# Kernel optimization log

Hardware: AMD Instinct MI355X
Metric: run time of the kernel (lower is better)

## Reference

```python
import jax, jax.numpy as jnp
import numpy as np

N_NODES = 100000


def _gcn_layer(x, src, dst, nrm, W, b):
    # x: [N, Din] -> [N, Dout]. GCNConv: linear transform then deg-normalized scatter-add.
    h = x @ W                                  # [N, Dout]
    msg = h[src] * nrm[:, None]               # gather + per-edge normalization, [E', Dout]
    agg = jax.ops.segment_sum(msg, dst, num_segments=N_NODES)
    return agg + b


def setup_inputs() -> dict:
    key = jax.random.key(0)
    ks = jax.random.split(key, 16)
    x = jax.random.normal(ks[0], (N_NODES, 128), dtype=jnp.float32)
    edge_index = jax.random.randint(ks[1], (2, 1600000), 0, N_NODES, dtype=jnp.int64)
    d = {"x": x, "edge_index": edge_index}
    dims = [(128, 64), (64, 64), (64, 64), (64, 64), (64, 64), (64, 64)]
    for i, (din, dout) in enumerate(dims):
        scale = 1.0 / np.sqrt(din)
        d[f"W{i+1}"] = jax.random.uniform(ks[2 + 2 * i], (din, dout), jnp.float32, -scale, scale)
        d[f"b{i+1}"] = jnp.zeros((dout,), jnp.float32)
    return d


def reference(x, edge_index, W1, b1, W2, b2, W3, b3, W4, b4, W5, b5, W6, b6):
    # Add self-loops (GCNConv default), symmetric normalization D^-1/2 A D^-1/2.
    loops = jnp.arange(N_NODES, dtype=edge_index.dtype)
    src = jnp.concatenate([edge_index[0], loops])
    dst = jnp.concatenate([edge_index[1], loops])
    deg = jax.ops.segment_sum(jnp.ones_like(dst, dtype=x.dtype), dst, num_segments=N_NODES)
    dinv = jnp.where(deg > 0, jax.lax.rsqrt(deg), 0.0)
    nrm = dinv[src] * dinv[dst]               # per-edge norm coefficient, [E']

    h = x
    for (W, b) in ((W1, b1), (W2, b2), (W3, b3), (W4, b4), (W5, b5), (W6, b6)):
        h = jax.nn.relu(_gcn_layer(h, src, dst, nrm, W, b))
        # eval mode: dropout is identity
    return jax.nn.log_softmax(h, axis=-1)
```

## Files before the change

### kernel.cpp

```cpp
#include <hip/hip_runtime.h>
#include <hip/hip_fp16.h>
#include <math.h>

#define N_NODES 100000
#define N_EDGES 1600000
#define NB 1563
#define CAP 2048
#define NBLK_S 128
#define CHUNK (N_EDGES / NBLK_S)

typedef _Float16 half8_t __attribute__((ext_vector_type(8)));
typedef float floatx4 __attribute__((ext_vector_type(4)));


__global__ __launch_bounds__(1024) void k_hist(const int* __restrict__ dst,
                                               int* __restrict__ ghist) {
    __shared__ int hist[NB];
    int blk = blockIdx.x, t = threadIdx.x;
    for (int i = t; i < NB; i += 1024) hist[i] = 0;
    __syncthreads();
    const int4* dq = (const int4*)(dst + blk * CHUNK);
    const int nq = CHUNK >> 2;
    for (int i = t; i < nq; i += 1024) {
        int4 d = dq[i];
        atomicAdd(&hist[d.x >> 6], 1);
        atomicAdd(&hist[d.y >> 6], 1);
        atomicAdd(&hist[d.z >> 6], 1);
        atomicAdd(&hist[d.w >> 6], 1);
    }
    __syncthreads();
    for (int i = t; i < NB; i += 1024) ghist[i * NBLK_S + blk] = hist[i];
}

__global__ void k_scanb(int* __restrict__ ghist, int* __restrict__ btot) {
    __shared__ int s[NBLK_S];
    int b = blockIdx.x, t = threadIdx.x;
    int v = ghist[b * NBLK_S + t];
    s[t] = v;
    __syncthreads();
    for (int off = 1; off < NBLK_S; off <<= 1) {
        int a = (t >= off) ? s[t - off] : 0;
        __syncthreads();
        s[t] += a;
        __syncthreads();
    }
    ghist[b * NBLK_S + t] = s[t] - v;
    if (t == NBLK_S - 1) btot[b] = s[t];
}

__global__ void k_scant(const int* __restrict__ btot, int* __restrict__ bbase,
                        int* __restrict__ rowptr) {
    __shared__ int s[1024];
    __shared__ int carry;
    int t = threadIdx.x;
    if (t == 0) carry = 0;
    __syncthreads();
    for (int chunk = 0; chunk < 2; ++chunk) {
        int i = chunk * 1024 + t;
        int v = (i < NB) ? btot[i] : 0;
        s[t] = v;
        __syncthreads();
        for (int off = 1; off < 1024; off <<= 1) {
            int a = (t >= off) ? s[t - off] : 0;
            __syncthreads();
            s[t] += a;
            __syncthreads();
        }
        if (i < NB) bbase[i] = carry + s[t] - v;
        int total = carry + s[1023];
        __syncthreads();
        if (t == 0) carry = total;
        __syncthreads();
    }
    if (t == 0) rowptr[N_NODES] = N_EDGES;
}

__global__ __launch_bounds__(1024) void k_scatter(const int* __restrict__ src,
                                                  const int* __restrict__ dst,
                                                  const int* __restrict__ ghist,
                                                  const int* __restrict__ bbase,
                                                  unsigned* __restrict__ bentry) {
    __shared__ int cursor[NB];
    int blk = blockIdx.x, t = threadIdx.x;
    for (int i = t; i < NB; i += 1024)
        cursor[i] = bbase[i] + ghist[i * NBLK_S + blk];
    __syncthreads();
    const int4* dq = (const int4*)(dst + blk * CHUNK);
    const int4* sq = (const int4*)(src + blk * CHUNK);
    const int nq = CHUNK >> 2;
    for (int i = t; i < nq; i += 1024) {
        int4 d = dq[i];
        int4 s = sq[i];
        int p0 = atomicAdd(&cursor[d.x >> 6], 1);
        int p1 = atomicAdd(&cursor[d.y >> 6], 1);
        int p2 = atomicAdd(&cursor[d.z >> 6], 1);
        int p3 = atomicAdd(&cursor[d.w >> 6], 1);
        bentry[p0] = ((unsigned)(d.x & 63) << 17) | (unsigned)s.x;
        bentry[p1] = ((unsigned)(d.y & 63) << 17) | (unsigned)s.y;
        bentry[p2] = ((unsigned)(d.z & 63) << 17) | (unsigned)s.z;
        bentry[p3] = ((unsigned)(d.w & 63) << 17) | (unsigned)s.w;
    }
}

__global__ __launch_bounds__(256) void k_fill2(const int* __restrict__ btot,
                                               const int* __restrict__ bbase,
                                               const unsigned* __restrict__ bentry,
                                               int* __restrict__ rowptr,
                                               float* __restrict__ dinv,
                                               int* __restrict__ colv) {
    __shared__ unsigned ent[CAP];
    __shared__ int hist[64];
    __shared__ int cursor[64];
    int b = blockIdx.x;
    int t = threadIdx.x;
    int cnt = btot[b]; if (cnt > CAP) cnt = CAP;
    int base = bbase[b];
    if (t < 64) hist[t] = 0;
    __syncthreads();
    const unsigned* be = bentry + base;
    for (int i = t; i < cnt; i += 256) {
        unsigned e = be[i];
        ent[i] = e;
        atomicAdd(&hist[e >> 17], 1);
    }
    __syncthreads();
    if (t < 64) {
        int v = hist[t];
        int incl = v;
#pragma unroll
        for (int off = 1; off < 64; off <<= 1) {
            int a = __shfl_up(incl, off);
            if (t >= off) incl += a;
        }
        int excl = incl - v;
        cursor[t] = excl;
        int node = (b << 6) + t;
        if (node < N_NODES) {
            rowptr[node] = base + excl;
            dinv[node] = rsqrtf((float)(v + 1));
        }
    }
    __syncthreads();
    for (int i = t; i < cnt; i += 256) {
        unsigned e = ent[i];
        int pos = base + atomicAdd(&cursor[e >> 17], 1);
        colv[pos] = (int)(e & 0x1FFFF);
    }
}


__global__ void k_prepw(const float* __restrict__ W1, const float* __restrict__ W2,
                        const float* __restrict__ W3, const float* __restrict__ W4,
                        const float* __restrict__ W5, const float* __restrict__ W6,
                        __half* __restrict__ wt) {
    int l = blockIdx.x;
    const float* W = (l == 0) ? W1 : (l == 1) ? W2 : (l == 2) ? W3
                   : (l == 3) ? W4 : (l == 4) ? W5 : W6;
    int din = (l == 0) ? 128 : 64;
    __half* dstp = wt + ((l == 0) ? 0 : 8192 + (l - 1) * 4096);
    int n = 64 * din;
    for (int i = threadIdx.x; i < n; i += blockDim.x) {
        int col = i / din, k = i - col * din;
        dstp[i] = __float2half(W[k * 64 + col]);
    }
}


template<int DIN, int F32IN>
__global__ __launch_bounds__(256) void k_gemm(const void* __restrict__ in,
                                              const __half* __restrict__ Wt,
                                              const float* __restrict__ dinv,
                                              __half* __restrict__ h) {
    int tid  = threadIdx.x;
    int lane = tid & 63;
    int node0 = blockIdx.x * 64 + (tid >> 6) * 16;
    if (node0 >= N_NODES) return;
    int lr = lane & 15;
    int lk = (lane >> 4) * 8;

    int arow = node0 + lr; if (arow >= N_NODES) arow = N_NODES - 1;
    const __half* ap  = (const __half*)in + (size_t)arow * DIN + lk;
    const float*  ap32 = (const float*)in + (size_t)arow * DIN + lk;
    const __half* bp = Wt + (size_t)lr * DIN + lk;

    floatx4 acc0 = {0.f, 0.f, 0.f, 0.f}, acc1 = acc0, acc2 = acc0, acc3 = acc0;
#pragma unroll
    for (int kc = 0; kc < DIN / 32; ++kc) {
        half8_t a;
        if (F32IN) {
            float4 f0 = *(const float4*)(ap32 + kc * 32);
            float4 f1 = *(const float4*)(ap32 + kc * 32 + 4);
            a[0] = (_Float16)f0.x; a[1] = (_Float16)f0.y;
            a[2] = (_Float16)f0.z; a[3] = (_Float16)f0.w;
            a[4] = (_Float16)f1.x; a[5] = (_Float16)f1.y;
            a[6] = (_Float16)f1.z; a[7] = (_Float16)f1.w;
        } else {
            a = *(const half8_t*)(ap + kc * 32);
        }
        half8_t b0 = *(const half8_t*)(bp + kc * 32);
        half8_t b1 = *(const half8_t*)(bp + kc * 32 + 16 * DIN);
        half8_t b2 = *(const half8_t*)(bp + kc * 32 + 32 * DIN);
        half8_t b3 = *(const half8_t*)(bp + kc * 32 + 48 * DIN);
        acc0 = __builtin_amdgcn_mfma_f32_16x16x32_f16(a, b0, acc0, 0, 0, 0);
        acc1 = __builtin_amdgcn_mfma_f32_16x16x32_f16(a, b1, acc1, 0, 0, 0);
        acc2 = __builtin_amdgcn_mfma_f32_16x16x32_f16(a, b2, acc2, 0, 0, 0);
        acc3 = __builtin_amdgcn_mfma_f32_16x16x32_f16(a, b3, acc3, 0, 0, 0);
    }

    int rbase = node0 + (lane >> 4) * 4;
#pragma unroll
    for (int r = 0; r < 4; ++r) {
        int row = rbase + r;
        if (row < N_NODES) {
            float dn = dinv[row];
            __half* op = h + ((size_t)row << 6) + lr;
            op[0]  = __float2half(acc0[r] * dn);
            op[16] = __float2half(acc1[r] * dn);
            op[32] = __float2half(acc2[r] * dn);
            op[48] = __float2half(acc3[r] * dn);
        }
    }
}


template<int LAST>
__global__ __launch_bounds__(256) void k_aggregate(const int* __restrict__ rowptr,
                                                   const int* __restrict__ colv,
                                                   const __half* __restrict__ h,
                                                   const float* __restrict__ dinv,
                                                   const float* __restrict__ bias,
                                                   __half* __restrict__ acta,
                                                   float* __restrict__ outf) {
    int tid  = threadIdx.x;
    int node = blockIdx.x * 16 + (tid >> 4);
    if (node >= N_NODES) return;
    int ql = tid & 15;

    int beg = rowptr[node], end = rowptr[node + 1];
    const __half* hp = h + (ql << 2);

    __half2 z = __floats2half2_rn(0.f, 0.f);
    __half2 A0 = z, A1 = z, B0 = z, B1 = z, C0 = z, C1 = z, D0 = z, D1 = z;
    union UV { uint2 u; __half2 h2[2]; };
    int k = beg;
    for (; k + 8 <= end; k += 8) {
        int s0 = colv[k],     s1 = colv[k + 1], s2 = colv[k + 2], s3 = colv[k + 3];
        int s4 = colv[k + 4], s5 = colv[k + 5], s6 = colv[k + 6], s7 = colv[k + 7];
        UV v0, v1, v2, v3, v4, v5, v6, v7;
        v0.u = *(const uint2*)(hp + ((size_t)s0 << 6));
        v1.u = *(const uint2*)(hp + ((size_t)s1 << 6));
        v2.u = *(const uint2*)(hp + ((size_t)s2 << 6));
        v3.u = *(const uint2*)(hp + ((size_t)s3 << 6));
        v4.u = *(const uint2*)(hp + ((size_t)s4 << 6));
        v5.u = *(const uint2*)(hp + ((size_t)s5 << 6));
        v6.u = *(const uint2*)(hp + ((size_t)s6 << 6));
        v7.u = *(const uint2*)(hp + ((size_t)s7 << 6));
        A0 = __hadd2(A0, v0.h2[0]); A1 = __hadd2(A1, v0.h2[1]);
        B0 = __hadd2(B0, v1.h2[0]); B1 = __hadd2(B1, v1.h2[1]);
        C0 = __hadd2(C0, v2.h2[0]); C1 = __hadd2(C1, v2.h2[1]);
        D0 = __hadd2(D0, v3.h2[0]); D1 = __hadd2(D1, v3.h2[1]);
        A0 = __hadd2(A0, v4.h2[0]); A1 = __hadd2(A1, v4.h2[1]);
        B0 = __hadd2(B0, v5.h2[0]); B1 = __hadd2(B1, v5.h2[1]);
        C0 = __hadd2(C0, v6.h2[0]); C1 = __hadd2(C1, v6.h2[1]);
        D0 = __hadd2(D0, v7.h2[0]); D1 = __hadd2(D1, v7.h2[1]);
    }
    for (; k + 4 <= end; k += 4) {
        int s0 = colv[k], s1 = colv[k + 1], s2 = colv[k + 2], s3 = colv[k + 3];
        UV v0, v1, v2, v3;
        v0.u = *(const uint2*)(hp + ((size_t)s0 << 6));
        v1.u = *(const uint2*)(hp + ((size_t)s1 << 6));
        v2.u = *(const uint2*)(hp + ((size_t)s2 << 6));
        v3.u = *(const uint2*)(hp + ((size_t)s3 << 6));
        A0 = __hadd2(A0, v0.h2[0]); A1 = __hadd2(A1, v0.h2[1]);
        B0 = __hadd2(B0, v1.h2[0]); B1 = __hadd2(B1, v1.h2[1]);
        C0 = __hadd2(C0, v2.h2[0]); C1 = __hadd2(C1, v2.h2[1]);
        D0 = __hadd2(D0, v3.h2[0]); D1 = __hadd2(D1, v3.h2[1]);
    }
    for (; k < end; ++k) {
        int s0 = colv[k];
        UV v0;
        v0.u = *(const uint2*)(hp + ((size_t)s0 << 6));
        A0 = __hadd2(A0, v0.h2[0]); A1 = __hadd2(A1, v0.h2[1]);
    }
    A0 = __hadd2(__hadd2(A0, B0), __hadd2(C0, D0));
    A1 = __hadd2(__hadd2(A1, B1), __hadd2(C1, D1));

    float2 f0 = __half22float2(A0), f1 = __half22float2(A1);
    UV sv;
    sv.u = *(const uint2*)(hp + ((size_t)node << 6));
    float2 s0f = __half22float2(sv.h2[0]), s1f = __half22float2(sv.h2[1]);
    float dn = dinv[node];
    float4 bv = ((const float4*)bias)[ql];
    float r0 = fmaxf(fmaf(f0.x + s0f.x, dn, bv.x), 0.f);
    float r1 = fmaxf(fmaf(f0.y + s0f.y, dn, bv.y), 0.f);
    float r2 = fmaxf(fmaf(f1.x + s1f.x, dn, bv.z), 0.f);
    float r3 = fmaxf(fmaf(f1.y + s1f.y, dn, bv.w), 0.f);

    if (LAST) {
        float m = fmaxf(fmaxf(r0, r1), fmaxf(r2, r3));
#pragma unroll
        for (int off = 1; off <= 8; off <<= 1) m = fmaxf(m, __shfl_xor(m, off));
        float ss = expf(r0 - m) + expf(r1 - m) + expf(r2 - m) + expf(r3 - m);
#pragma unroll
        for (int off = 1; off <= 8; off <<= 1) ss += __shfl_xor(ss, off);
        float lse = m + logf(ss);
        *(float4*)(outf + ((size_t)node << 6) + (ql << 2)) =
            make_float4(r0 - lse, r1 - lse, r2 - lse, r3 - lse);
    } else {
        UV pk;
        pk.h2[0] = __floats2half2_rn(r0, r1);
        pk.h2[1] = __floats2half2_rn(r2, r3);
        *(uint2*)(acta + ((size_t)node << 6) + (ql << 2)) = pk.u;
    }
}


extern "C" void kernel_launch(void* const* d_in, const int* in_sizes, int n_in,
                              void* d_out, int out_size, void* d_ws, size_t ws_size,
                              hipStream_t stream) {
    const float* x = (const float*)d_in[0];
    const int* ei  = (const int*)d_in[1];
    const int* src = ei;
    const int* dst = ei + N_EDGES;

    const float* W[6];
    const float* b[6];
    for (int i = 0; i < 6; ++i) {
        W[i] = (const float*)d_in[2 + 2 * i];
        b[i] = (const float*)d_in[3 + 2 * i];
    }
    float* out = (float*)d_out;

    char* p = (char*)d_ws;
    __half* h      = (__half*)p; p += (size_t)N_NODES * 64 * 2;
    __half* act    = (__half*)p; p += (size_t)N_NODES * 64 * 2;
    __half* wt     = (__half*)p; p += 28672 * 2;
    int*    rowptr = (int*)p;    p += (size_t)(N_NODES + 1) * 4;
    float*  dinv   = (float*)p;  p += (size_t)N_NODES * 4;
    int*    colv   = (int*)p;
    unsigned* bentry = (unsigned*)h;
    int*    ghist = (int*)(bentry + (size_t)N_EDGES);
    int*    btot  = ghist + (size_t)NB * NBLK_S;
    int*    bbase = btot + NB;

    const int nb_q    = (N_NODES + 15) / 16;
    const int nb_tile = (N_NODES + 63) / 64;

    k_prepw<<<6, 256, 0, stream>>>(W[0], W[1], W[2], W[3], W[4], W[5], wt);

    k_hist<<<NBLK_S, 1024, 0, stream>>>(dst, ghist);
    k_scanb<<<NB, NBLK_S, 0, stream>>>(ghist, btot);
    k_scant<<<1, 1024, 0, stream>>>(btot, bbase, rowptr);
    k_scatter<<<NBLK_S, 1024, 0, stream>>>(src, dst, ghist, bbase, bentry);
    k_fill2<<<NB, 256, 0, stream>>>(btot, bbase, bentry, rowptr, dinv, colv);

    for (int l = 0; l < 6; ++l) {
        if (l == 0)
            k_gemm<128, 1><<<nb_tile, 256, 0, stream>>>(x, wt, dinv, h);
        else
            k_gemm<64, 0><<<nb_tile, 256, 0, stream>>>(act, wt + 8192 + (l - 1) * 4096, dinv, h);
        if (l == 5)
            k_aggregate<1><<<nb_q, 256, 0, stream>>>(rowptr, colv, h, dinv, b[l], act, out);
        else
            k_aggregate<0><<<nb_q, 256, 0, stream>>>(rowptr, colv, h, dinv, b[l], act, out);
    }
}
```

Before: 351.5 us.

## Fuse aggregation of layer l with GEMM of layer l+1 via LDS tile

Each layer's neighbor aggregation (with bias, ReLU and fp16 packing) now writes a 64-node tile into shared memory, and the next layer's MFMA GEMM reads it from there, all in one kernel. This drops the intermediate activation write/read through global memory and five kernel launches, using ping-pong h buffers. The cost is fewer, larger blocks (64 nodes each, 4 serial node rows per 16-lane group), which lowers parallelism for latency hiding in the gather.

Result: slower. 366.8 us (+4.4%).

```diff
diff --git a/kernel.cpp b/kernel.cpp
--- a/kernel.cpp
+++ b/kernel.cpp
@@ -166,11 +166,10 @@
 }
 
 
-template<int DIN, int F32IN>
-__global__ __launch_bounds__(256) void k_gemm(const void* __restrict__ in,
-                                              const __half* __restrict__ Wt,
-                                              const float* __restrict__ dinv,
-                                              __half* __restrict__ h) {
+__global__ __launch_bounds__(256) void k_gemm0(const float* __restrict__ in,
+                                               const __half* __restrict__ Wt,
+                                               const float* __restrict__ dinv,
+                                               __half* __restrict__ h) {
     int tid  = threadIdx.x;
     int lane = tid & 63;
     int node0 = blockIdx.x * 64 + (tid >> 6) * 16;
@@ -179,28 +178,23 @@
     int lk = (lane >> 4) * 8;
 
     int arow = node0 + lr; if (arow >= N_NODES) arow = N_NODES - 1;
-    const __half* ap  = (const __half*)in + (size_t)arow * DIN + lk;
-    const float*  ap32 = (const float*)in + (size_t)arow * DIN + lk;
-    const __half* bp = Wt + (size_t)lr * DIN + lk;
+    const float*  ap32 = in + (size_t)arow * 128 + lk;
+    const __half* bp = Wt + (size_t)lr * 128 + lk;
 
     floatx4 acc0 = {0.f, 0.f, 0.f, 0.f}, acc1 = acc0, acc2 = acc0, acc3 = acc0;
 #pragma unroll
-    for (int kc = 0; kc < DIN / 32; ++kc) {
+    for (int kc = 0; kc < 4; ++kc) {
+        float4 f0 = *(const float4*)(ap32 + kc * 32);
+        float4 f1 = *(const float4*)(ap32 + kc * 32 + 4);
         half8_t a;
-        if (F32IN) {
-            float4 f0 = *(const float4*)(ap32 + kc * 32);
-            float4 f1 = *(const float4*)(ap32 + kc * 32 + 4);
-            a[0] = (_Float16)f0.x; a[1] = (_Float16)f0.y;
-            a[2] = (_Float16)f0.z; a[3] = (_Float16)f0.w;
-            a[4] = (_Float16)f1.x; a[5] = (_Float16)f1.y;
-            a[6] = (_Float16)f1.z; a[7] = (_Float16)f1.w;
-        } else {
-            a = *(const half8_t*)(ap + kc * 32);
-        }
+        a[0] = (_Float16)f0.x; a[1] = (_Float16)f0.y;
+        a[2] = (_Float16)f0.z; a[3] = (_Float16)f0.w;
+        a[4] = (_Float16)f1.x; a[5] = (_Float16)f1.y;
+        a[6] = (_Float16)f1.z; a[7] = (_Float16)f1.w;
         half8_t b0 = *(const half8_t*)(bp + kc * 32);
-        half8_t b1 = *(const half8_t*)(bp + kc * 32 + 16 * DIN);
-        half8_t b2 = *(const half8_t*)(bp + kc * 32 + 32 * DIN);
-        half8_t b3 = *(const half8_t*)(bp + kc * 32 + 48 * DIN);
+        half8_t b1 = *(const half8_t*)(bp + kc * 32 + 16 * 128);
+        half8_t b2 = *(const half8_t*)(bp + kc * 32 + 32 * 128);
+        half8_t b3 = *(const half8_t*)(bp + kc * 32 + 48 * 128);
         acc0 = __builtin_amdgcn_mfma_f32_16x16x32_f16(a, b0, acc0, 0, 0, 0);
         acc1 = __builtin_amdgcn_mfma_f32_16x16x32_f16(a, b1, acc1, 0, 0, 0);
         acc2 = __builtin_amdgcn_mfma_f32_16x16x32_f16(a, b2, acc2, 0, 0, 0);
@@ -223,14 +217,130 @@
 }
 
 
-template<int LAST>
-__global__ __launch_bounds__(256) void k_aggregate(const int* __restrict__ rowptr,
-                                                   const int* __restrict__ colv,
-                                                   const __half* __restrict__ h,
-                                                   const float* __restrict__ dinv,
-                                                   const float* __restrict__ bias,
-                                                   __half* __restrict__ acta,
-                                                   float* __restrict__ outf) {
+__global__ __launch_bounds__(256) void k_fused(const int* __restrict__ rowptr,
+                                               const int* __restrict__ colv,
+                                               const __half* __restrict__ h,
+                                               const float* __restrict__ dinv,
+                                               const float* __restrict__ bias,
+                                               const __half* __restrict__ Wt,
+                                               __half* __restrict__ hn) {
+    __shared__ __half sA[64 * 80];
+    int tid = threadIdx.x;
+    int node0 = blockIdx.x * 64;
+    int q = tid >> 4, ql = tid & 15;
+    const __half* hp = h + (ql << 2);
+    float4 bv = ((const float4*)bias)[ql];
+    union UV { uint2 u; __half2 h2[2]; };
+
+    for (int j = 0; j < 4; ++j) {
+        int trow = (j << 4) + q;
+        int node = node0 + trow;
+        uint2* sdst = (uint2*)&sA[trow * 80 + (ql << 2)];
+        if (node >= N_NODES) { *sdst = make_uint2(0u, 0u); continue; }
+        int beg = rowptr[node], end = rowptr[node + 1];
+        __half2 z = __floats2half2_rn(0.f, 0.f);
+        __half2 A0 = z, A1 = z, B0 = z, B1 = z, C0 = z, C1 = z, D0 = z, D1 = z;
+        int k = beg;
+        for (; k + 8 <= end; k += 8) {
+            int s0 = colv[k],     s1 = colv[k + 1], s2 = colv[k + 2], s3 = colv[k + 3];
+            int s4 = colv[k + 4], s5 = colv[k + 5], s6 = colv[k + 6], s7 = colv[k + 7];
+            UV v0, v1, v2, v3, v4, v5, v6, v7;
+            v0.u = *(const uint2*)(hp + ((size_t)s0 << 6));
+            v1.u = *(const uint2*)(hp + ((size_t)s1 << 6));
+            v2.u = *(const uint2*)(hp + ((size_t)s2 << 6));
+            v3.u = *(const uint2*)(hp + ((size_t)s3 << 6));
+            v4.u = *(const uint2*)(hp + ((size_t)s4 << 6));
+            v5.u = *(const uint2*)(hp + ((size_t)s5 << 6));
+            v6.u = *(const uint2*)(hp + ((size_t)s6 << 6));
+            v7.u = *(const uint2*)(hp + ((size_t)s7 << 6));
+            A0 = __hadd2(A0, v0.h2[0]); A1 = __hadd2(A1, v0.h2[1]);
+            B0 = __hadd2(B0, v1.h2[0]); B1 = __hadd2(B1, v1.h2[1]);
+            C0 = __hadd2(C0, v2.h2[0]); C1 = __hadd2(C1, v2.h2[1]);
+            D0 = __hadd2(D0, v3.h2[0]); D1 = __hadd2(D1, v3.h2[1]);
+            A0 = __hadd2(A0, v4.h2[0]); A1 = __hadd2(A1, v4.h2[1]);
+            B0 = __hadd2(B0, v5.h2[0]); B1 = __hadd2(B1, v5.h2[1]);
+            C0 = __hadd2(C0, v6.h2[0]); C1 = __hadd2(C1, v6.h2[1]);
+            D0 = __hadd2(D0, v7.h2[0]); D1 = __hadd2(D1, v7.h2[1]);
+        }
+        for (; k + 4 <= end; k += 4) {
+            int s0 = colv[k], s1 = colv[k + 1], s2 = colv[k + 2], s3 = colv[k + 3];
+            UV v0, v1, v2, v3;
+            v0.u = *(const uint2*)(hp + ((size_t)s0 << 6));
+            v1.u = *(const uint2*)(hp + ((size_t)s1 << 6));
+            v2.u = *(const uint2*)(hp + ((size_t)s2 << 6));
+            v3.u = *(const uint2*)(hp + ((size_t)s3 << 6));
+            A0 = __hadd2(A0, v0.h2[0]); A1 = __hadd2(A1, v0.h2[1]);
+            B0 = __hadd2(B0, v1.h2[0]); B1 = __hadd2(B1, v1.h2[1]);
+            C0 = __hadd2(C0, v2.h2[0]); C1 = __hadd2(C1, v2.h2[1]);
+            D0 = __hadd2(D0, v3.h2[0]); D1 = __hadd2(D1, v3.h2[1]);
+        }
+        for (; k < end; ++k) {
+            int s0 = colv[k];
+            UV v0;
+            v0.u = *(const uint2*)(hp + ((size_t)s0 << 6));
+            A0 = __hadd2(A0, v0.h2[0]); A1 = __hadd2(A1, v0.h2[1]);
+        }
+        A0 = __hadd2(__hadd2(A0, B0), __hadd2(C0, D0));
+        A1 = __hadd2(__hadd2(A1, B1), __hadd2(C1, D1));
+
+        float2 f0 = __half22float2(A0), f1 = __half22float2(A1);
+        UV sv;
+        sv.u = *(const uint2*)(hp + ((size_t)node << 6));
+        float2 s0f = __half22float2(sv.h2[0]), s1f = __half22float2(sv.h2[1]);
+        float dn = dinv[node];
+        float r0 = fmaxf(fmaf(f0.x + s0f.x, dn, bv.x), 0.f);
+        float r1 = fmaxf(fmaf(f0.y + s0f.y, dn, bv.y), 0.f);
+        float r2 = fmaxf(fmaf(f1.x + s1f.x, dn, bv.z), 0.f);
+        float r3 = fmaxf(fmaf(f1.y + s1f.y, dn, bv.w), 0.f);
+        UV pk;
+        pk.h2[0] = __floats2half2_rn(r0, r1);
+        pk.h2[1] = __floats2half2_rn(r2, r3);
+        *sdst = pk.u;
+    }
+    __syncthreads();
+
+    int lane = tid & 63;
+    int lr = lane & 15;
+    int lk = (lane >> 4) * 8;
+    int wrow0 = (tid >> 6) * 16;
+    const __half* bp = Wt + (size_t)lr * 64 + lk;
+
+    floatx4 acc0 = {0.f, 0.f, 0.f, 0.f}, acc1 = acc0, acc2 = acc0, acc3 = acc0;
+#pragma unroll
+    for (int kc = 0; kc < 2; ++kc) {
+        half8_t a  = *(const half8_t*)&sA[(wrow0 + lr) * 80 + kc * 32 + lk];
+        half8_t b0 = *(const half8_t*)(bp + kc * 32);
+        half8_t b1 = *(const half8_t*)(bp + kc * 32 + 16 * 64);
+        half8_t b2 = *(const half8_t*)(bp + kc * 32 + 32 * 64);
+        half8_t b3 = *(const half8_t*)(bp + kc * 32 + 48 * 64);
+        acc0 = __builtin_amdgcn_mfma_f32_16x16x32_f16(a, b0, acc0, 0, 0, 0);
+        acc1 = __builtin_amdgcn_mfma_f32_16x16x32_f16(a, b1, acc1, 0, 0, 0);
+        acc2 = __builtin_amdgcn_mfma_f32_16x16x32_f16(a, b2, acc2, 0, 0, 0);
+        acc3 = __builtin_amdgcn_mfma_f32_16x16x32_f16(a, b3, acc3, 0, 0, 0);
+    }
+
+    int rbase = node0 + wrow0 + (lane >> 4) * 4;
+#pragma unroll
+    for (int r = 0; r < 4; ++r) {
+        int row = rbase + r;
+        if (row < N_NODES) {
+            float dn = dinv[row];
+            __half* op = hn + ((size_t)row << 6) + lr;
+            op[0]  = __float2half(acc0[r] * dn);
+            op[16] = __float2half(acc1[r] * dn);
+            op[32] = __float2half(acc2[r] * dn);
+            op[48] = __float2half(acc3[r] * dn);
+        }
+    }
+}
+
+
+__global__ __launch_bounds__(256) void k_aggsm(const int* __restrict__ rowptr,
+                                               const int* __restrict__ colv,
+                                               const __half* __restrict__ h,
+                                               const float* __restrict__ dinv,
+                                               const float* __restrict__ bias,
+                                               float* __restrict__ outf) {
     int tid  = threadIdx.x;
     int node = blockIdx.x * 16 + (tid >> 4);
     if (node >= N_NODES) return;
@@ -296,22 +406,15 @@
     float r2 = fmaxf(fmaf(f1.x + s1f.x, dn, bv.z), 0.f);
     float r3 = fmaxf(fmaf(f1.y + s1f.y, dn, bv.w), 0.f);
 
-    if (LAST) {
-        float m = fmaxf(fmaxf(r0, r1), fmaxf(r2, r3));
-#pragma unroll
-        for (int off = 1; off <= 8; off <<= 1) m = fmaxf(m, __shfl_xor(m, off));
-        float ss = expf(r0 - m) + expf(r1 - m) + expf(r2 - m) + expf(r3 - m);
-#pragma unroll
-        for (int off = 1; off <= 8; off <<= 1) ss += __shfl_xor(ss, off);
-        float lse = m + logf(ss);
-        *(float4*)(outf + ((size_t)node << 6) + (ql << 2)) =
-            make_float4(r0 - lse, r1 - lse, r2 - lse, r3 - lse);
-    } else {
-        UV pk;
-        pk.h2[0] = __floats2half2_rn(r0, r1);
-        pk.h2[1] = __floats2half2_rn(r2, r3);
-        *(uint2*)(acta + ((size_t)node << 6) + (ql << 2)) = pk.u;
-    }
+    float m = fmaxf(fmaxf(r0, r1), fmaxf(r2, r3));
+#pragma unroll
+    for (int off = 1; off <= 8; off <<= 1) m = fmaxf(m, __shfl_xor(m, off));
+    float ss = expf(r0 - m) + expf(r1 - m) + expf(r2 - m) + expf(r3 - m);
+#pragma unroll
+    for (int off = 1; off <= 8; off <<= 1) ss += __shfl_xor(ss, off);
+    float lse = m + logf(ss);
+    *(float4*)(outf + ((size_t)node << 6) + (ql << 2)) =
+        make_float4(r0 - lse, r1 - lse, r2 - lse, r3 - lse);
 }
 
 
@@ -332,13 +435,13 @@
     float* out = (float*)d_out;
 
     char* p = (char*)d_ws;
-    __half* h      = (__half*)p; p += (size_t)N_NODES * 64 * 2;
-    __half* act    = (__half*)p; p += (size_t)N_NODES * 64 * 2;
+    __half* hA     = (__half*)p; p += (size_t)N_NODES * 64 * 2;
+    __half* hB     = (__half*)p; p += (size_t)N_NODES * 64 * 2;
     __half* wt     = (__half*)p; p += 28672 * 2;
     int*    rowptr = (int*)p;    p += (size_t)(N_NODES + 1) * 4;
     float*  dinv   = (float*)p;  p += (size_t)N_NODES * 4;
     int*    colv   = (int*)p;
-    unsigned* bentry = (unsigned*)h;
+    unsigned* bentry = (unsigned*)hA;
     int*    ghist = (int*)(bentry + (size_t)N_EDGES);
     int*    btot  = ghist + (size_t)NB * NBLK_S;
     int*    bbase = btot + NB;
@@ -354,14 +457,13 @@
     k_scatter<<<NBLK_S, 1024, 0, stream>>>(src, dst, ghist, bbase, bentry);
     k_fill2<<<NB, 256, 0, stream>>>(btot, bbase, bentry, rowptr, dinv, colv);
 
-    for (int l = 0; l < 6; ++l) {
-        if (l == 0)
-            k_gemm<128, 1><<<nb_tile, 256, 0, stream>>>(x, wt, dinv, h);
-        else
-            k_gemm<64, 0><<<nb_tile, 256, 0, stream>>>(act, wt + 8192 + (l - 1) * 4096, dinv, h);
-        if (l == 5)
-            k_aggregate<1><<<nb_q, 256, 0, stream>>>(rowptr, colv, h, dinv, b[l], act, out);
-        else
-            k_aggregate<0><<<nb_q, 256, 0, stream>>>(rowptr, colv, h, dinv, b[l], act, out);
-    }
-}
+    k_gemm0<<<nb_tile, 256, 0, stream>>>(x, wt, dinv, hA);
+    __half* hc = hA;
+    __half* hn = hB;
+    for (int l = 1; l <= 5; ++l) {
+        k_fused<<<nb_tile, 256, 0, stream>>>(rowptr, colv, hc, dinv, b[l - 1],
+                                             wt + 8192 + (l - 1) * 4096, hn);
+        __half* tswap = hc; hc = hn; hn = tswap;
+    }
+    k_aggsm<<<nb_q, 256, 0, stream>>>(rowptr, colv, hc, dinv, b[5], out);
+}
```
